# Optimization experiments

Hardware: AMD Instinct MI355X
Metric: run time of the kernel (lower is better)

Reference implementation:

```python
import jax, jax.numpy as jnp
import numpy as np

EPS = 1e-6
NUM_HEADS = 16


def _layer_norm(x):
    # LayerNorm32: fp32 layernorm, eps=1e-6, no affine params
    m = jnp.mean(x, axis=-1, keepdims=True)
    v = jnp.var(x, axis=-1, keepdims=True)
    return (x - m) * jax.lax.rsqrt(v + EPS)


def setup_inputs() -> dict:
    key = jax.random.key(0)
    ks = jax.random.split(key, 6)
    B, L, C = 4, 2048, 1024
    H = 4 * C
    s = 0.02
    return {
        "x": jax.random.normal(ks[0], (B, L, C), dtype=jnp.float32),
        "qkv_w": jax.random.normal(ks[1], (C, 3 * C), dtype=jnp.float32) * s,
        "qkv_b": jnp.zeros((3 * C,), dtype=jnp.float32),
        "proj_w": jax.random.normal(ks[2], (C, C), dtype=jnp.float32) * s,
        "proj_b": jnp.zeros((C,), dtype=jnp.float32),
        "fc1_w": jax.random.normal(ks[3], (C, H), dtype=jnp.float32) * s,
        "fc1_b": jnp.zeros((H,), dtype=jnp.float32),
        "fc2_w": jax.random.normal(ks[4], (H, C), dtype=jnp.float32) * s,
        "fc2_b": jnp.zeros((C,), dtype=jnp.float32),
    }


def _block(x, qkv_w, qkv_b, proj_w, proj_b, fc1_w, fc1_b, fc2_w, fc2_b):
    B, L, C = x.shape
    Hn = NUM_HEADS
    D = C // Hn

    # --- attention branch (pre-norm) ---
    h = _layer_norm(x)
    qkv = h @ qkv_w + qkv_b                      # [B, L, 3C]
    qkv = qkv.reshape(B, L, 3, Hn, D)
    q, k, v = qkv[:, :, 0], qkv[:, :, 1], qkv[:, :, 2]  # [B, L, Hn, D]
    scale = 1.0 / jnp.sqrt(jnp.asarray(D, dtype=x.dtype))
    logits = jnp.einsum("bqhd,bkhd->bhqk", q, k) * scale
    attn = jax.nn.softmax(logits, axis=-1)
    o = jnp.einsum("bhqk,bkhd->bqhd", attn, v).reshape(B, L, C)
    o = o @ proj_w + proj_b
    x = x + o

    # --- MLP branch (pre-norm) ---
    h = _layer_norm(x)
    h = jax.nn.gelu(h @ fc1_w + fc1_b, approximate=True)  # tanh GELU
    h = h @ fc2_w + fc2_b
    return x + h


def reference(x, qkv_w, qkv_b, proj_w, proj_b, fc1_w, fc1_b, fc2_w, fc2_b):
    return _block(x, qkv_w, qkv_b, proj_w, proj_b, fc1_w, fc1_b, fc2_w, fc2_b)
```

## Files before the change

kernel.cpp:

```cpp
#include <hip/hip_runtime.h>
#include <hip/hip_bf16.h>

typedef float f32x4 __attribute__((ext_vector_type(4)));
typedef __bf16 bf16x8 __attribute__((ext_vector_type(8)));
typedef unsigned short us8 __attribute__((ext_vector_type(8)));

#define MBYTE (1ull << 20)

#define QSCALE_LOG2E 0.18033688011112042f
#define GELU_K 2.3022081902f

__device__ __forceinline__ unsigned short f2bf(float f) {
    __bf16 h = (__bf16)f;
    return __builtin_bit_cast(unsigned short, h);
}

__device__ __forceinline__ float fast_exp2(float x) {
    return __builtin_amdgcn_exp2f(x);
}

__device__ __forceinline__ f32x4 mfma16(bf16x8 a, bf16x8 b, f32x4 c) {
    return __builtin_amdgcn_mfma_f32_16x16x32_bf16(a, b, c, 0, 0, 0);
}

__device__ __forceinline__ void gload16(const void* g, void* l) {
    __builtin_amdgcn_global_load_lds(
        (const __attribute__((address_space(1))) unsigned int*)g,
        (__attribute__((address_space(3))) unsigned int*)l, 16, 0, 0);
}

__global__ __launch_bounds__(256) void ln_kernel(const float* __restrict__ x,
                                                 unsigned short* __restrict__ out) {
    int row = blockIdx.x;
    int t = threadIdx.x;
    const float* xr = x + (size_t)row * 1024;
    float4 v = *(const float4*)(xr + t * 4);
    float s = v.x + v.y + v.z + v.w;
    float ss = v.x * v.x + v.y * v.y + v.z * v.z + v.w * v.w;
    #pragma unroll
    for (int off = 1; off < 64; off <<= 1) {
        s += __shfl_xor(s, off);
        ss += __shfl_xor(ss, off);
    }
    __shared__ float ps[4], pss[4];
    int wid = t >> 6, lane = t & 63;
    if (lane == 0) { ps[wid] = s; pss[wid] = ss; }
    __syncthreads();
    s = ps[0] + ps[1] + ps[2] + ps[3];
    ss = pss[0] + pss[1] + pss[2] + pss[3];
    float mean = s * (1.0f / 1024.0f);
    float var = ss * (1.0f / 1024.0f) - mean * mean;
    float rs = rsqrtf(var + 1e-6f);
    ushort4 ov;
    ov.x = f2bf((v.x - mean) * rs);
    ov.y = f2bf((v.y - mean) * rs);
    ov.z = f2bf((v.z - mean) * rs);
    ov.w = f2bf((v.w - mean) * rs);
    *(ushort4*)(out + (size_t)row * 1024 + t * 4) = ov;
}

__global__ __launch_bounds__(256) void convT_kernel(const float* __restrict__ W,
                                                    unsigned short* __restrict__ Wt,
                                                    int K, int N) {
    __shared__ float tile[32][33];
    int t = threadIdx.x;
    int tx = t & 31, ty = t >> 5;
    int bx = blockIdx.x, by = blockIdx.y;
    #pragma unroll
    for (int r = 0; r < 4; r++) {
        int row = by * 32 + ty + r * 8;
        int col = bx * 32 + tx;
        tile[ty + r * 8][tx] = W[(size_t)row * N + col];
    }
    __syncthreads();
    #pragma unroll
    for (int r = 0; r < 4; r++) {
        int orow = bx * 32 + ty + r * 8;
        int ocol = by * 32 + tx;
        Wt[(size_t)orow * K + ocol] = f2bf(tile[tx][ty + r * 8]);
    }
}

__global__ __launch_bounds__(256) void vT_kernel(const unsigned short* __restrict__ qkv,
                                                 unsigned short* __restrict__ vT) {
    __shared__ unsigned short tile[32][34];
    int t = threadIdx.x;
    int tx = t & 31, ty = t >> 5;
    int lt = blockIdx.x, dt = blockIdx.y, bh = blockIdx.z;
    int b = bh >> 4, h = bh & 15;
    const unsigned short* src = qkv + (size_t)(b * 2048 + lt * 32) * 3072 + 2048 + h * 64 + dt * 32;
    #pragma unroll
    for (int r = 0; r < 4; r++)
        tile[ty + r * 8][tx] = src[(size_t)(ty + r * 8) * 3072 + tx];
    __syncthreads();
    int perm = (lt & 1) * 32 + ((tx >> 2) & 3) * 8 + ((tx >> 4) & 1) * 4 + (tx & 3);
    unsigned short* dst = vT + ((size_t)bh * 64 + dt * 32) * 2048 + (size_t)(lt >> 1) * 64;
    #pragma unroll
    for (int r = 0; r < 4; r++)
        dst[(size_t)(ty + r * 8) * 2048 + perm] = tile[tx][ty + r * 8];
}

template <int EPI>
__global__ __launch_bounds__(256) void gemm_bt(const unsigned short* __restrict__ A,
                                               const unsigned short* __restrict__ Bt,
                                               const float* __restrict__ bias,
                                               const float* __restrict__ res,
                                               float* __restrict__ outF,
                                               unsigned short* __restrict__ outB,
                                               int M, int N, int K) {
    __shared__ __align__(16) unsigned short As[2][128 * 32];
    __shared__ __align__(16) unsigned short Bs[2][128 * 32];
    int t = threadIdx.x;
    int lane = t & 63, wid = t >> 6;

    int gx = gridDim.x;
    int nwg = gx * gridDim.y;
    int orig = blockIdx.y * gx + blockIdx.x;
    int cpx = nwg >> 3;
    int swz = (orig & 7) * cpx + (orig >> 3);
    int bm = swz / gx, bn = swz % gx;

    int wm = wid >> 1, wn = wid & 1;
    f32x4 acc[4][4] = {};

    int sub = lane >> 2;
    int schunk = ((lane & 3) ^ ((lane >> 3) & 3)) * 8;
    const unsigned short* gA0 = A + (size_t)(bm * 128 + wid * 32 + sub) * K + schunk;
    const unsigned short* gA1 = gA0 + (size_t)16 * K;
    const unsigned short* gB0 = Bt + (size_t)(bn * 128 + wid * 32 + sub) * K + schunk;
    const unsigned short* gB1 = gB0 + (size_t)16 * K;

    int ql = lane & 15;
    int rchunk = (((lane >> 4) ^ ((lane >> 1) & 3))) * 8;

    const int NT = K >> 5;
    gload16(gA0, &As[0][(wid * 32) * 32]);
    gload16(gA1, &As[0][(wid * 32 + 16) * 32]);
    gload16(gB0, &Bs[0][(wid * 32) * 32]);
    gload16(gB1, &Bs[0][(wid * 32 + 16) * 32]);
    __syncthreads();

    int cur = 0;
    for (int tt = 0; tt < NT; ++tt) {
        if (tt + 1 < NT) {
            int k0 = (tt + 1) << 5;
            int nb = cur ^ 1;
            gload16(gA0 + k0, &As[nb][(wid * 32) * 32]);
            gload16(gA1 + k0, &As[nb][(wid * 32 + 16) * 32]);
            gload16(gB0 + k0, &Bs[nb][(wid * 32) * 32]);
            gload16(gB1 + k0, &Bs[nb][(wid * 32 + 16) * 32]);
        }
        bf16x8 af[4], bfr[4];
        #pragma unroll
        for (int m = 0; m < 4; m++)
            af[m] = *(const bf16x8*)&As[cur][(wm * 64 + m * 16 + ql) * 32 + rchunk];
        #pragma unroll
        for (int n = 0; n < 4; n++)
            bfr[n] = *(const bf16x8*)&Bs[cur][(wn * 64 + n * 16 + ql) * 32 + rchunk];
        __builtin_amdgcn_s_setprio(1);
        #pragma unroll
        for (int m = 0; m < 4; m++)
            #pragma unroll
            for (int n = 0; n < 4; n++)
                acc[m][n] = mfma16(af[m], bfr[n], acc[m][n]);
        __builtin_amdgcn_s_setprio(0);
        __syncthreads();
        cur ^= 1;
    }

    #pragma unroll
    for (int m = 0; m < 4; m++) {
        #pragma unroll
        for (int n = 0; n < 4; n++) {
            int col = bn * 128 + wn * 64 + n * 16 + ql;
            float bv = bias[col];
            #pragma unroll
            for (int r = 0; r < 4; r++) {
                int row = bm * 128 + wm * 64 + m * 16 + (lane >> 4) * 4 + r;
                float val = acc[m][n][r] + bv;
                if (EPI == 0) {
                    if (col < 1024) val *= QSCALE_LOG2E;
                    outB[(size_t)row * N + col] = f2bf(val);
                } else if (EPI == 1) {
                    float w = val + 0.044715f * val * val * val;
                    float g = val / (1.0f + fast_exp2(-GELU_K * w));
                    outB[(size_t)row * N + col] = f2bf(g);
                } else {
                    outF[(size_t)row * N + col] = val + res[(size_t)row * N + col];
                }
            }
        }
    }
}

__global__ __launch_bounds__(256) void attn_kernel(const unsigned short* __restrict__ qkv,
                                                   const unsigned short* __restrict__ vT,
                                                   unsigned short* __restrict__ o) {
    int bid = blockIdx.x;
    int qb = bid & 31;
    int bh = bid >> 5;
    int b = bh >> 4, h = bh & 15;
    int t = threadIdx.x, lane = t & 63, wid = t >> 6;

    const unsigned short* base = qkv + (size_t)b * 2048 * 3072 + h * 64;
    const unsigned short* vbase = vT + (size_t)bh * 64 * 2048;

    __shared__ __align__(16) unsigned short Ks[2][64][32];
    __shared__ __align__(16) unsigned short Vs[2][64][32];

    int ql = lane & 15;
    int hi = lane >> 4;

    bf16x8 qf[2];
    {
        int qrow = qb * 64 + wid * 16 + ql;
        const unsigned short* qp = base + (size_t)qrow * 3072 + hi * 8;
        qf[0] = *(const bf16x8*)(qp);
        qf[1] = *(const bf16x8*)(qp + 32);
    }

    float m_r = -1e30f, lpart = 0.0f;
    f32x4 accO[4] = {};

    int srow = wid * 16 + (lane >> 2);
    int schunk = ((lane & 3) ^ ((lane >> 3) & 3)) * 8;
    const unsigned short* gk = base + 1024 + (size_t)srow * 3072 + schunk;
    const unsigned short* gv = vbase + (size_t)srow * 2048 + schunk;
    unsigned short* lK0 = &Ks[0][wid * 16][0];
    unsigned short* lK1 = &Ks[1][wid * 16][0];
    unsigned short* lV0 = &Vs[0][wid * 16][0];
    unsigned short* lV1 = &Vs[1][wid * 16][0];

    int rchunk = (hi ^ ((ql >> 1) & 3)) * 8;

    for (int kt = 0; kt < 32; kt++) {
        __syncthreads();
        gload16(gk, lK0);
        gload16(gk + 32, lK1);
        gload16(gv, lV0);
        gload16(gv + 32, lV1);
        gk += (size_t)64 * 3072;
        gv += 64;
        __syncthreads();

        f32x4 s0 = {}, s1 = {}, s2 = {}, s3 = {};
        #pragma unroll
        for (int c = 0; c < 2; c++) {
            bf16x8 a0 = *(const bf16x8*)&Ks[c][ 0 + ql][rchunk];
            bf16x8 a1 = *(const bf16x8*)&Ks[c][16 + ql][rchunk];
            bf16x8 a2 = *(const bf16x8*)&Ks[c][32 + ql][rchunk];
            bf16x8 a3 = *(const bf16x8*)&Ks[c][48 + ql][rchunk];
            s0 = mfma16(a0, qf[c], s0);
            s1 = mfma16(a1, qf[c], s1);
            s2 = mfma16(a2, qf[c], s2);
            s3 = mfma16(a3, qf[c], s3);
        }

        float mx = fmaxf(fmaxf(fmaxf(s0[0], s0[1]), fmaxf(s0[2], s0[3])),
                         fmaxf(fmaxf(s1[0], s1[1]), fmaxf(s1[2], s1[3])));
        mx = fmaxf(mx, fmaxf(fmaxf(s2[0], s2[1]), fmaxf(s2[2], s2[3])));
        mx = fmaxf(mx, fmaxf(fmaxf(s3[0], s3[1]), fmaxf(s3[2], s3[3])));
        if (!__all(mx <= m_r + 8.0f)) {
            float mm = fmaxf(mx, __shfl_xor(mx, 16));
            mm = fmaxf(mm, __shfl_xor(mm, 32));
            float mnew = fmaxf(m_r, mm);
            float corr = fast_exp2(m_r - mnew);
            m_r = mnew;
            lpart *= corr;
            #pragma unroll
            for (int r = 0; r < 4; r++) {
                float cq = __shfl(corr, hi * 4 + r);
                accO[0][r] *= cq; accO[1][r] *= cq;
                accO[2][r] *= cq; accO[3][r] *= cq;
            }
        }

        us8 pu0, pu1;
        #pragma unroll
        for (int j = 0; j < 4; j++) {
            float pa = fast_exp2(s0[j] - m_r);
            float pb = fast_exp2(s1[j] - m_r);
            float pc = fast_exp2(s2[j] - m_r);
            float pd = fast_exp2(s3[j] - m_r);
            lpart += (pa + pb) + (pc + pd);
            pu0[j] = f2bf(pa); pu0[4 + j] = f2bf(pb);
            pu1[j] = f2bf(pc); pu1[4 + j] = f2bf(pd);
        }
        bf16x8 paf0 = __builtin_bit_cast(bf16x8, pu0);
        bf16x8 paf1 = __builtin_bit_cast(bf16x8, pu1);

        #pragma unroll
        for (int nn = 0; nn < 4; nn++) {
            bf16x8 bv0 = *(const bf16x8*)&Vs[0][nn * 16 + ql][rchunk];
            bf16x8 bv1 = *(const bf16x8*)&Vs[1][nn * 16 + ql][rchunk];
            accO[nn] = mfma16(paf0, bv0, accO[nn]);
            accO[nn] = mfma16(paf1, bv1, accO[nn]);
        }
    }

    lpart += __shfl_xor(lpart, 16);
    lpart += __shfl_xor(lpart, 32);
    float rinv = 1.0f / lpart;
    #pragma unroll
    for (int r = 0; r < 4; r++) {
        float rq = __shfl(rinv, hi * 4 + r);
        int row = qb * 64 + wid * 16 + hi * 4 + r;
        #pragma unroll
        for (int nn = 0; nn < 4; nn++) {
            int col = h * 64 + nn * 16 + ql;
            o[(size_t)(b * 2048 + row) * 1024 + col] = f2bf(accO[nn][r] * rq);
        }
    }
}

extern "C" void kernel_launch(void* const* d_in, const int* in_sizes, int n_in,
                              void* d_out, int out_size, void* d_ws, size_t ws_size,
                              hipStream_t stream) {
    const float* x      = (const float*)d_in[0];
    const float* qkv_w  = (const float*)d_in[1];
    const float* qkv_b  = (const float*)d_in[2];
    const float* proj_w = (const float*)d_in[3];
    const float* proj_b = (const float*)d_in[4];
    const float* fc1_w  = (const float*)d_in[5];
    const float* fc1_b  = (const float*)d_in[6];
    const float* fc2_w  = (const float*)d_in[7];
    const float* fc2_b  = (const float*)d_in[8];
    float* out = (float*)d_out;

    char* ws = (char*)d_ws;
    unsigned short* h_buf   = (unsigned short*)(ws + 0 * MBYTE);
    unsigned short* qkv_buf = (unsigned short*)(ws + 16 * MBYTE);
    unsigned short* o_buf   = (unsigned short*)(ws + 64 * MBYTE);
    float*          x2_buf  = (float*)(ws + 80 * MBYTE);
    unsigned short* vT_buf  = (unsigned short*)(ws + 80 * MBYTE);
    unsigned short* wqT     = (unsigned short*)(ws + 112 * MBYTE);
    unsigned short* wpT     = (unsigned short*)(ws + 118 * MBYTE);
    unsigned short* w1T     = (unsigned short*)(ws + 120 * MBYTE);
    unsigned short* w2T     = (unsigned short*)(ws + 128 * MBYTE);
    unsigned short* g_buf   = (unsigned short*)(ws + 16 * MBYTE);

    const int M = 8192;

    convT_kernel<<<dim3(3072 / 32, 1024 / 32), 256, 0, stream>>>(qkv_w, wqT, 1024, 3072);
    convT_kernel<<<dim3(1024 / 32, 1024 / 32), 256, 0, stream>>>(proj_w, wpT, 1024, 1024);
    convT_kernel<<<dim3(4096 / 32, 1024 / 32), 256, 0, stream>>>(fc1_w, w1T, 1024, 4096);
    convT_kernel<<<dim3(1024 / 32, 4096 / 32), 256, 0, stream>>>(fc2_w, w2T, 4096, 1024);

    ln_kernel<<<M, 256, 0, stream>>>(x, h_buf);

    gemm_bt<0><<<dim3(3072 / 128, M / 128), 256, 0, stream>>>(
        h_buf, wqT, qkv_b, nullptr, nullptr, qkv_buf, M, 3072, 1024);

    vT_kernel<<<dim3(64, 2, 64), 256, 0, stream>>>(qkv_buf, vT_buf);

    attn_kernel<<<dim3(32 * 64), 256, 0, stream>>>(qkv_buf, vT_buf, o_buf);

    gemm_bt<2><<<dim3(1024 / 128, M / 128), 256, 0, stream>>>(
        o_buf, wpT, proj_b, x, x2_buf, nullptr, M, 1024, 1024);

    ln_kernel<<<M, 256, 0, stream>>>(x2_buf, h_buf);

    gemm_bt<1><<<dim3(4096 / 128, M / 128), 256, 0, stream>>>(
        h_buf, w1T, fc1_b, nullptr, nullptr, g_buf, M, 4096, 1024);

    gemm_bt<2><<<dim3(1024 / 128, M / 128), 256, 0, stream>>>(
        g_buf, w2T, fc2_b, x2_buf, out, nullptr, M, 1024, 4096);
}
```

Baseline: 448.7 us.

## Double-buffer K/V tiles in attention kernel to overlap loads with compute

The attention kernel now keeps two LDS buffers for K and V and prefetches the next key tile with direct-to-LDS loads while computing on the current one. Two __syncthreads per iteration become a single vmcnt wait plus barrier at the end of each iteration. This hides global load latency behind the MFMA and softmax work, at the cost of doubling the LDS footprint (16KB per block), which may reduce occupancy. The attention kernel is only one part of the full block, so the effect on total time is diluted.

```diff
diff --git a/kernel.cpp b/kernel.cpp
--- a/kernel.cpp
+++ b/kernel.cpp
@@ -205,8 +205,8 @@
     const unsigned short* base = qkv + (size_t)b * 2048 * 3072 + h * 64;
     const unsigned short* vbase = vT + (size_t)bh * 64 * 2048;
 
-    __shared__ __align__(16) unsigned short Ks[2][64][32];
-    __shared__ __align__(16) unsigned short Vs[2][64][32];
+    __shared__ __align__(16) unsigned short Ks[2][2][64][32];
+    __shared__ __align__(16) unsigned short Vs[2][2][64][32];
 
     int ql = lane & 15;
     int hi = lane >> 4;
@@ -226,30 +226,34 @@
     int schunk = ((lane & 3) ^ ((lane >> 3) & 3)) * 8;
     const unsigned short* gk = base + 1024 + (size_t)srow * 3072 + schunk;
     const unsigned short* gv = vbase + (size_t)srow * 2048 + schunk;
-    unsigned short* lK0 = &Ks[0][wid * 16][0];
-    unsigned short* lK1 = &Ks[1][wid * 16][0];
-    unsigned short* lV0 = &Vs[0][wid * 16][0];
-    unsigned short* lV1 = &Vs[1][wid * 16][0];
+
+    auto STAGE = [&](int buf, int kt) {
+        const unsigned short* pk = gk + (size_t)kt * 64 * 3072;
+        const unsigned short* pv = gv + (size_t)kt * 64;
+        gload16(pk, &Ks[buf][0][wid * 16][0]);
+        gload16(pk + 32, &Ks[buf][1][wid * 16][0]);
+        gload16(pv, &Vs[buf][0][wid * 16][0]);
+        gload16(pv + 32, &Vs[buf][1][wid * 16][0]);
+    };
 
     int rchunk = (hi ^ ((ql >> 1) & 3)) * 8;
 
+    STAGE(0, 0);
+    asm volatile("s_waitcnt vmcnt(0)" ::: "memory");
+    __builtin_amdgcn_sched_barrier(0);
+    __builtin_amdgcn_s_barrier();
+
+    int buf = 0;
     for (int kt = 0; kt < 32; kt++) {
-        __syncthreads();
-        gload16(gk, lK0);
-        gload16(gk + 32, lK1);
-        gload16(gv, lV0);
-        gload16(gv + 32, lV1);
-        gk += (size_t)64 * 3072;
-        gv += 64;
-        __syncthreads();
+        if (kt + 1 < 32) STAGE(buf ^ 1, kt + 1);
 
         f32x4 s0 = {}, s1 = {}, s2 = {}, s3 = {};
         #pragma unroll
         for (int c = 0; c < 2; c++) {
-            bf16x8 a0 = *(const bf16x8*)&Ks[c][ 0 + ql][rchunk];
-            bf16x8 a1 = *(const bf16x8*)&Ks[c][16 + ql][rchunk];
-            bf16x8 a2 = *(const bf16x8*)&Ks[c][32 + ql][rchunk];
-            bf16x8 a3 = *(const bf16x8*)&Ks[c][48 + ql][rchunk];
+            bf16x8 a0 = *(const bf16x8*)&Ks[buf][c][ 0 + ql][rchunk];
+            bf16x8 a1 = *(const bf16x8*)&Ks[buf][c][16 + ql][rchunk];
+            bf16x8 a2 = *(const bf16x8*)&Ks[buf][c][32 + ql][rchunk];
+            bf16x8 a3 = *(const bf16x8*)&Ks[buf][c][48 + ql][rchunk];
             s0 = mfma16(a0, qf[c], s0);
             s1 = mfma16(a1, qf[c], s1);
             s2 = mfma16(a2, qf[c], s2);
@@ -291,11 +295,16 @@
 
         #pragma unroll
         for (int nn = 0; nn < 4; nn++) {
-            bf16x8 bv0 = *(const bf16x8*)&Vs[0][nn * 16 + ql][rchunk];
-            bf16x8 bv1 = *(const bf16x8*)&Vs[1][nn * 16 + ql][rchunk];
+            bf16x8 bv0 = *(const bf16x8*)&Vs[buf][0][nn * 16 + ql][rchunk];
+            bf16x8 bv1 = *(const bf16x8*)&Vs[buf][1][nn * 16 + ql][rchunk];
             accO[nn] = mfma16(paf0, bv0, accO[nn]);
             accO[nn] = mfma16(paf1, bv1, accO[nn]);
         }
+
+        asm volatile("s_waitcnt vmcnt(0)" ::: "memory");
+        __builtin_amdgcn_sched_barrier(0);
+        __builtin_amdgcn_s_barrier();
+        buf ^= 1;
     }
 
     lpart += __shfl_xor(lpart, 16);
```

Measured after the change: 453.4 us. Within noise of the previous version (+1.0%).
